# Kernel tuning notes

Measured on AMD Instinct MI355X. Metric: run time of the kernel, lower is better.

Reference implementation:

```python
import jax, jax.numpy as jnp
import numpy as np

EPS = 1e-6
NUM_GROUPS = 32


def group_norm(x, w, b):
    # x: [B, C, W, H, L]
    B, C = x.shape[0], x.shape[1]
    xr = x.reshape(B, NUM_GROUPS, C // NUM_GROUPS, -1)
    mu = jnp.mean(xr, axis=(2, 3), keepdims=True)
    var = jnp.var(xr, axis=(2, 3), keepdims=True)
    xn = ((xr - mu) * jax.lax.rsqrt(var + EPS)).reshape(x.shape)
    return xn * w[None, :, None, None, None] + b[None, :, None, None, None]


def setup_inputs() -> dict:
    key = jax.random.key(0)
    ks = jax.random.split(key, 8)
    B, C, W, H, L = 2, 512, 16, 16, 16
    s = 1.0 / np.sqrt(C)
    return {
        "x": jax.random.normal(ks[0], (B, C, W, H, L), dtype=jnp.float32),
        "gn_w": jnp.ones((C,), dtype=jnp.float32),
        "gn_b": jnp.zeros((C,), dtype=jnp.float32),
        "q_w": jax.random.normal(ks[1], (C, C), dtype=jnp.float32) * s,
        "q_b": jnp.zeros((C,), dtype=jnp.float32),
        "k_w": jax.random.normal(ks[2], (C, C), dtype=jnp.float32) * s,
        "k_b": jnp.zeros((C,), dtype=jnp.float32),
        "v_w": jax.random.normal(ks[3], (C, C), dtype=jnp.float32) * s,
        "v_b": jnp.zeros((C,), dtype=jnp.float32),
        "p_w": jax.random.normal(ks[4], (C, C), dtype=jnp.float32) * s,
        "p_b": jnp.zeros((C,), dtype=jnp.float32),
    }


def reference(x, gn_w, gn_b, q_w, q_b, k_w, k_b, v_w, v_b, p_w, p_b):
    B, C, W, H, L = x.shape
    h = group_norm(x, gn_w, gn_b)
    hf = h.reshape(B, C, -1)  # [B, C, N]
    # 1x1 Conv3d == channel matmul: out[b,o,n] = sum_c w[o,c] * h[b,c,n] + b[o]
    q = jnp.einsum('oc,bcn->bon', q_w, hf) + q_b[None, :, None]
    k = jnp.einsum('oc,bcn->bon', k_w, hf) + k_b[None, :, None]
    v = jnp.einsum('oc,bcn->bon', v_w, hf) + v_b[None, :, None]
    scale = jnp.asarray(C, x.dtype) ** -0.5
    # w_[b,i,j] = sum_c q[b,c,i] * k[b,c,j]
    w_ = jnp.einsum('bci,bcj->bij', q, k) * scale
    w_ = jax.nn.softmax(w_, axis=2)
    # h_[b,c,i] = sum_j v[b,c,j] * w_[b,i,j]
    attn = jnp.einsum('bcj,bij->bci', v, w_)
    proj = jnp.einsum('oc,bcn->bon', p_w, attn) + p_b[None, :, None]
    return x + proj.reshape(B, C, W, H, L)
```

## Files before the change

### kernel.cpp

```cpp
#include <hip/hip_runtime.h>


typedef __bf16 bf16;
typedef __attribute__((ext_vector_type(8))) __bf16 bf16x8;
typedef __attribute__((ext_vector_type(4))) __bf16 bf16x4;
typedef __attribute__((ext_vector_type(4))) float f32x4;

#define CC 512
#define NN 4096
#define BM 128
#define BN 128
#define BK 64
#define SCALE_L2E 0.06376237870903338f

__device__ __forceinline__ void gload16(const bf16* g, bf16* l) {
    __builtin_amdgcn_global_load_lds(
        (const __attribute__((address_space(1))) unsigned int*)g,
        (__attribute__((address_space(3))) unsigned int*)l, 16, 0, 0);
}

template<int FA, int NSTEP>
__device__ __forceinline__ void core_p3(
    const bf16* __restrict__ A, int lda,
    const bf16* __restrict__ B, int ldb,
    int m0, int n0, f32x4 acc[FA][2])
{
    constexpr int BMt  = FA * 32;
    constexpr int ROWS = BMt + 128;
    constexpr int L    = ROWS / 64;
    __shared__ __align__(16) bf16 ls[3][ROWS][BK];

    const int t    = threadIdx.x;
    const int lane = t & 63;
    const int wid  = t >> 6;
    const int wm   = (wid >> 2) * (FA * 16);
    const int wn   = (wid & 3) * 32;
    const int fr   = lane & 15;
    const int kq   = lane >> 4;
    const int cs0  = ((kq)     ^ (fr & 7)) * 8;
    const int cs1  = ((kq + 4) ^ (fr & 7)) * 8;

    auto STAGE = [&](int bi, int kk) {
        #pragma unroll
        for (int j = 0; j < L; ++j) {
            const int idx = t + j * 512;
            const int row = idx >> 3;
            const int blk = (idx & 7) ^ (row & 7);
            const bf16* g = (row < BMt)
                ? A + (size_t)(m0 + row) * lda + kk + blk * 8
                : B + (size_t)(n0 + row - BMt) * ldb + kk + blk * 8;
            gload16(g, &ls[bi][row][(idx & 7) * 8]);
        }
    };

    STAGE(0, 0);
    STAGE(1, BK);
    for (int i = 0; i < NSTEP; ++i) {
        if (i + 2 < NSTEP) {
            STAGE((i + 2) % 3, (i + 2) * BK);
            asm volatile("s_waitcnt vmcnt(%0)" :: "n"(2 * L) : "memory");
        } else if (i + 1 < NSTEP) {
            asm volatile("s_waitcnt vmcnt(%0)" :: "n"(L) : "memory");
        } else {
            asm volatile("s_waitcnt vmcnt(0)" ::: "memory");
        }
        __builtin_amdgcn_s_barrier();
        const int bi = i % 3;
        #pragma unroll
        for (int h = 0; h < 2; ++h) {
            const int cs = h ? cs1 : cs0;
            bf16x8 af[FA], bg[2];
            #pragma unroll
            for (int f = 0; f < FA; ++f)
                af[f] = *(const bf16x8*)&ls[bi][wm + f * 16 + fr][cs];
            #pragma unroll
            for (int g = 0; g < 2; ++g)
                bg[g] = *(const bf16x8*)&ls[bi][BMt + wn + g * 16 + fr][cs];
            #pragma unroll
            for (int fm = 0; fm < FA; ++fm)
                #pragma unroll
                for (int g = 0; g < 2; ++g)
                    acc[fm][g] = __builtin_amdgcn_mfma_f32_16x16x32_bf16(
                        af[fm], bg[g], acc[fm][g], 0, 0, 0);
        }
        __builtin_amdgcn_s_barrier();
    }
}

__device__ __forceinline__ void gemm_core(
    const bf16* __restrict__ A, int lda,
    const bf16* __restrict__ B, int ldb,
    int kBeg, int kEnd, int m0, int n0, f32x4 acc[4][4])
{
    __shared__ __align__(16) bf16 Als[2][BM][BK];
    __shared__ __align__(16) bf16 Bls[2][BN][BK];
    const int t    = threadIdx.x;
    const int lane = t & 63;
    const int wid  = t >> 6;
    const int wm   = (wid >> 1) * 64;
    const int wn   = (wid & 1) * 64;
    const int fr   = lane & 15;
    const int kq   = lane >> 4;
    const int r_   = t >> 3;
    const int cbs  = (t & 7) ^ (r_ & 7);
    const int dcol = (t & 7) * 8;
    const int cs0  = ((kq)     ^ (fr & 7)) * 8;
    const int cs1  = ((kq + 4) ^ (fr & 7)) * 8;

    const bf16* Ab = A + (size_t)(m0 + r_) * lda + cbs * 8;
    const bf16* Bb = B + (size_t)(n0 + r_) * ldb + cbs * 8;

#define STAGE_G(bufi, kk) do {                                              \
        _Pragma("unroll")                                                   \
        for (int i = 0; i < 4; ++i)                                         \
            gload16(Ab + (kk) + (size_t)(i * 32) * lda,                     \
                    &Als[bufi][i * 32 + r_][dcol]);                         \
        _Pragma("unroll")                                                   \
        for (int i = 0; i < 4; ++i)                                         \
            gload16(Bb + (kk) + (size_t)(i * 32) * ldb,                     \
                    &Bls[bufi][i * 32 + r_][dcol]);                         \
    } while (0)

    int cur = 0;
    STAGE_G(0, kBeg);
    __syncthreads();
    for (int k0 = kBeg; k0 < kEnd; k0 += BK) {
        if (k0 + BK < kEnd) STAGE_G(cur ^ 1, k0 + BK);
        #pragma unroll
        for (int h = 0; h < 2; ++h) {
            const int cs = h ? cs1 : cs0;
            bf16x8 af[4], bg[4];
            #pragma unroll
            for (int f = 0; f < 4; ++f) {
                af[f] = *(const bf16x8*)&Als[cur][wm + f * 16 + fr][cs];
                bg[f] = *(const bf16x8*)&Bls[cur][wn + f * 16 + fr][cs];
            }
            #pragma unroll
            for (int fm = 0; fm < 4; ++fm)
                #pragma unroll
                for (int fn = 0; fn < 4; ++fn)
                    acc[fm][fn] = __builtin_amdgcn_mfma_f32_16x16x32_bf16(
                        af[fm], bg[fn], acc[fm][fn], 0, 0, 0);
        }
        __syncthreads();
        cur ^= 1;
    }
#undef STAGE_G
}

__global__ __launch_bounds__(256) void convert_w_kernel(
    const float* __restrict__ qw, const float* __restrict__ kw,
    const float* __restrict__ pw, bf16* __restrict__ dst)
{
    const int which = blockIdx.y;
    const float* src = which == 0 ? qw : which == 1 ? kw : pw;
    const int slot  = which == 2 ? 3 : which;
    bf16* d = dst + (size_t)slot * (CC * CC);
    const int f4 = blockIdx.x * 256 + threadIdx.x;
    float4 v = ((const float4*)src)[f4];
    bf16x4 o;
    o[0] = (bf16)v.x; o[1] = (bf16)v.y; o[2] = (bf16)v.z; o[3] = (bf16)v.w;
    ((bf16x4*)d)[f4] = o;
}

__global__ __launch_bounds__(256) void vwT_kernel(
    const float* __restrict__ vw, bf16* __restrict__ vwT)
{
    const int k0 = blockIdx.x * 64;
    const int c0 = blockIdx.y * 64;
    const int t  = threadIdx.x;
    const int tk = t & 15, tc = t >> 4;
    float o[4][4];
    #pragma unroll
    for (int j = 0; j < 4; ++j) {
        const int c = c0 + tc * 4 + j;
        float4 v = *(const float4*)(vw + (size_t)c * CC + k0 + tk * 4);
        o[j][0] = v.x; o[j][1] = v.y; o[j][2] = v.z; o[j][3] = v.w;
    }
    #pragma unroll
    for (int i = 0; i < 4; ++i) {
        bf16x4 w4;
        w4[0] = (bf16)o[0][i]; w4[1] = (bf16)o[1][i];
        w4[2] = (bf16)o[2][i]; w4[3] = (bf16)o[3][i];
        *(bf16x4*)(vwT + (size_t)(k0 + tk * 4 + i) * CC + c0 + tc * 4) = w4;
    }
}

__global__ __launch_bounds__(256) void wb_kernel(
    const float* __restrict__ pw, const float* __restrict__ vb,
    float* __restrict__ wb)
{
    const int o = blockIdx.x * 256 + threadIdx.x;
    const float4* row = (const float4*)(pw + (size_t)o * CC);
    const float4* v4  = (const float4*)vb;
    float s = 0.f;
    #pragma unroll 4
    for (int i = 0; i < 128; ++i) {
        float4 a = row[i], b = v4[i];
        s += a.x * b.x + a.y * b.y + a.z * b.z + a.w * b.w;
    }
    wb[o] = s;
}

__global__ __launch_bounds__(256) void gn_stats_kernel(
    const float* __restrict__ x, float* __restrict__ mr)
{
    const int bg = blockIdx.x;
    const float4* base = (const float4*)(x + (size_t)bg * 16 * NN);
    const int t = threadIdx.x;
    float s = 0.f, sq = 0.f;
    #pragma unroll 4
    for (int i = 0; i < 64; ++i) {
        float4 v = base[i * 256 + t];
        s  += v.x + v.y + v.z + v.w;
        sq += v.x * v.x + v.y * v.y + v.z * v.z + v.w * v.w;
    }
    #pragma unroll
    for (int o = 32; o > 0; o >>= 1) { s += __shfl_xor(s, o); sq += __shfl_xor(sq, o); }
    __shared__ float rs[4], rq[4];
    const int lane = t & 63, wid = t >> 6;
    if (lane == 0) { rs[wid] = s; rq[wid] = sq; }
    __syncthreads();
    if (t == 0) {
        float S = rs[0] + rs[1] + rs[2] + rs[3];
        float Q = rq[0] + rq[1] + rq[2] + rq[3];
        const float invn = 1.f / 65536.f;
        float mean = S * invn;
        float var  = Q * invn - mean * mean;
        mr[bg * 2]     = mean;
        mr[bg * 2 + 1] = rsqrtf(var + 1e-6f);
    }
}

__global__ __launch_bounds__(256) void gn_apply_T_kernel(
    const float* __restrict__ x, const float* __restrict__ gw,
    const float* __restrict__ gb, const float* __restrict__ mr,
    bf16* __restrict__ hT)
{
    const int b  = blockIdx.z;
    const int n0 = blockIdx.x * 64;
    const int c0 = blockIdx.y * 64;
    const int t  = threadIdx.x;
    const int tn = t & 15, tc = t >> 4;
    float o[4][4];
    #pragma unroll
    for (int j = 0; j < 4; ++j) {
        const int c = c0 + tc * 4 + j;
        const int bg = b * 32 + (c >> 4);
        const float mean = mr[bg * 2], rstd = mr[bg * 2 + 1];
        const float w  = gw[c] * rstd;
        const float bb = gb[c] - mean * w;
        float4 v = *(const float4*)(x + ((size_t)(b * CC + c)) * NN + n0 + tn * 4);
        o[j][0] = v.x * w + bb; o[j][1] = v.y * w + bb;
        o[j][2] = v.z * w + bb; o[j][3] = v.w * w + bb;
    }
    bf16* dst = hT + (size_t)b * (size_t)NN * CC;
    #pragma unroll
    for (int i = 0; i < 4; ++i) {
        bf16x4 w4;
        w4[0] = (bf16)o[0][i]; w4[1] = (bf16)o[1][i];
        w4[2] = (bf16)o[2][i]; w4[3] = (bf16)o[3][i];
        *(bf16x4*)(dst + (size_t)(n0 + tn * 4 + i) * CC + c0 + tc * 4) = w4;
    }
}

__global__ __launch_bounds__(256) void fw_gemm_kernel(
    const bf16* __restrict__ pwb, const bf16* __restrict__ vwT,
    bf16* __restrict__ fw)
{
    const int m0 = blockIdx.y * BM, n0 = blockIdx.x * BN;
    f32x4 acc[4][4] = {};
    gemm_core(pwb, CC, vwT, CC, 0, CC, m0, n0, acc);
    const int lane = threadIdx.x & 63, wid = threadIdx.x >> 6;
    const int wm = (wid >> 1) * 64, wn = (wid & 1) * 64;
    const int cf = lane & 15, rb = (lane >> 4) * 4;
    #pragma unroll
    for (int fm = 0; fm < 4; ++fm)
      #pragma unroll
      for (int fn = 0; fn < 4; ++fn)
        #pragma unroll
        for (int r = 0; r < 4; ++r)
            fw[(size_t)(m0 + wm + fm * 16 + rb + r) * CC
               + (n0 + wn + fn * 16 + cf)] = (bf16)acc[fm][fn][r];
}

__global__ __launch_bounds__(512, 2) void qk_gemm_kernel(
    const bf16* __restrict__ hT, const bf16* __restrict__ wbf,
    const float* __restrict__ qb, const float* __restrict__ kb,
    bf16* __restrict__ qT, bf16* __restrict__ kT)
{
    const int z = blockIdx.z, b = z >> 1, w = z & 1;
    const size_t CN = (size_t)CC * NN;
    const bf16* A = hT + (size_t)b * CN;
    const bf16* B = wbf + (size_t)w * CC * CC;
    const float* bias = w ? kb : qb;
    bf16* outp = (w ? kT : qT) + (size_t)b * CN;
    const int m0 = blockIdx.y * 256, n0 = blockIdx.x * 128;
    f32x4 acc[8][2] = {};
    core_p3<8, CC / BK>(A, CC, B, CC, m0, n0, acc);
    const int lane = threadIdx.x & 63, wid = threadIdx.x >> 6;
    const int wm = (wid >> 2) * 128, wn = (wid & 3) * 32;
    const int cf = lane & 15, rb = (lane >> 4) * 4;
    #pragma unroll
    for (int fm = 0; fm < 8; ++fm)
      #pragma unroll
      for (int g = 0; g < 2; ++g)
        #pragma unroll
        for (int r = 0; r < 4; ++r) {
            int row = m0 + wm + fm * 16 + rb + r;
            int col = n0 + wn + g * 16 + cf;
            float val = acc[fm][g][r] + bias[col];
            if (w == 0) val *= SCALE_L2E;
            outp[(size_t)row * CC + col] = (bf16)val;
        }
}

__global__ __launch_bounds__(512, 2) void w_gemm_kernel(
    const bf16* __restrict__ fw, const bf16* __restrict__ hT,
    bf16* __restrict__ Wt)
{
    const int b = blockIdx.z;
    const size_t CN = (size_t)CC * NN;
    const int m0 = blockIdx.y * 128, n0 = blockIdx.x * 128;
    f32x4 acc[4][2] = {};
    core_p3<4, CC / BK>(fw, CC, hT + (size_t)b * CN, CC, m0, n0, acc);
    bf16* outp = Wt + (size_t)b * CN;
    const int lane = threadIdx.x & 63, wid = threadIdx.x >> 6;
    const int wm = (wid >> 2) * 64, wn = (wid & 3) * 32;
    const int cf = lane & 15, rb = (lane >> 4) * 4;
    #pragma unroll
    for (int fm = 0; fm < 4; ++fm)
      #pragma unroll
      for (int g = 0; g < 2; ++g)
        #pragma unroll
        for (int r = 0; r < 4; ++r)
            outp[(size_t)(m0 + wm + fm * 16 + rb + r) * NN
                 + (n0 + wn + g * 16 + cf)] = (bf16)acc[fm][g][r];
}

__global__ __launch_bounds__(512, 2) void se_gemm_kernel(
    const bf16* __restrict__ qT, const bf16* __restrict__ kT,
    bf16* __restrict__ E, float* __restrict__ rowsum)
{
    const int b = blockIdx.z;
    const size_t CN = (size_t)CC * NN;
    const bf16* qT_b = qT + (size_t)b * CN;
    const bf16* kT_b = kT + (size_t)b * CN;
    bf16* E_b = E + (size_t)b * NN * NN;
    float* rs_b = rowsum + (size_t)b * NN;
    const int m0 = blockIdx.y * 256, n0 = blockIdx.x * 128;
    f32x4 acc[8][2] = {};
    core_p3<8, CC / BK>(qT_b, CC, kT_b, CC, m0, n0, acc);
    const int lane = threadIdx.x & 63, wid = threadIdx.x >> 6;
    const int wm = (wid >> 2) * 128, wn = (wid & 3) * 32;
    const int cf = lane & 15, rb = (lane >> 4) * 4;
    #pragma unroll
    for (int fm = 0; fm < 8; ++fm)
      #pragma unroll
      for (int g = 0; g < 2; ++g)
        #pragma unroll
        for (int r = 0; r < 4; ++r) {
            float e = exp2f(fminf(acc[fm][g][r], 86.f));
            acc[fm][g][r] = e;
            E_b[(size_t)(m0 + wm + fm * 16 + rb + r) * NN
                + (n0 + wn + g * 16 + cf)] = (bf16)e;
        }
    #pragma unroll
    for (int fm = 0; fm < 8; ++fm)
      #pragma unroll
      for (int r = 0; r < 4; ++r) {
          float s = acc[fm][0][r] + acc[fm][1][r];
          s += __shfl_xor(s, 1); s += __shfl_xor(s, 2);
          s += __shfl_xor(s, 4); s += __shfl_xor(s, 8);
          if (cf == 0)
              atomicAdd(&rs_b[m0 + wm + fm * 16 + rb + r], s);
      }
}

__global__ __launch_bounds__(512, 2) void pvproj_kernel(
    const bf16* __restrict__ Wt, const bf16* __restrict__ E,
    const float* __restrict__ rowsum, const float* __restrict__ wb,
    const float* __restrict__ pb, const float* __restrict__ x,
    float* __restrict__ outp)
{
    const int b = blockIdx.z;
    const size_t CN = (size_t)CC * NN;
    const int m0 = blockIdx.y * 128, n0 = blockIdx.x * 128;
    f32x4 acc[4][2] = {};
    core_p3<4, NN / BK>(Wt + (size_t)b * CN, NN,
                        E + (size_t)b * NN * NN, NN, m0, n0, acc);
    const float* rs_b = rowsum + (size_t)b * NN;
    const int lane = threadIdx.x & 63, wid = threadIdx.x >> 6;
    const int wm = (wid >> 2) * 64, wn = (wid & 3) * 32;
    const int cf = lane & 15, rb = (lane >> 4) * 4;
    #pragma unroll
    for (int fm = 0; fm < 4; ++fm)
      #pragma unroll
      for (int g = 0; g < 2; ++g) {
          const int col = n0 + wn + g * 16 + cf;
          const float inv = 1.f / rs_b[col];
          #pragma unroll
          for (int r = 0; r < 4; ++r) {
              const int row = m0 + wm + fm * 16 + rb + r;
              const size_t idx = (size_t)b * CN + (size_t)row * NN + col;
              outp[idx] = acc[fm][g][r] * inv + wb[row] + pb[row] + x[idx];
          }
      }
}

extern "C" void kernel_launch(void* const* d_in, const int* in_sizes, int n_in,
                              void* d_out, int out_size, void* d_ws, size_t ws_size,
                              hipStream_t stream)
{
    const float* x   = (const float*)d_in[0];
    const float* gnw = (const float*)d_in[1];
    const float* gnb = (const float*)d_in[2];
    const float* qw  = (const float*)d_in[3];
    const float* qb  = (const float*)d_in[4];
    const float* kw  = (const float*)d_in[5];
    const float* kb  = (const float*)d_in[6];
    const float* vw  = (const float*)d_in[7];
    const float* vb  = (const float*)d_in[8];
    const float* pw  = (const float*)d_in[9];
    const float* pb  = (const float*)d_in[10];
    float* outp = (float*)d_out;

    char* ws = (char*)d_ws;
    size_t off = 0;
    auto alloc = [&](size_t bytes) -> char* {
        char* p = ws + off;
        off = (off + bytes + 255) & ~(size_t)255;
        return p;
    };
    const size_t CN = (size_t)CC * NN;
    bf16*  wbf  = (bf16*)alloc(4 * (size_t)CC * CC * sizeof(bf16));
    bf16*  hT   = (bf16*)alloc(2 * CN * sizeof(bf16));
    bf16*  qT   = (bf16*)alloc(2 * CN * sizeof(bf16));
    bf16*  kT   = (bf16*)alloc(2 * CN * sizeof(bf16));
    bf16*  fw   = (bf16*)alloc((size_t)CC * CC * sizeof(bf16));
    bf16*  Wt   = (bf16*)alloc(2 * CN * sizeof(bf16));
    bf16*  E    = (bf16*)alloc(2 * (size_t)NN * NN * sizeof(bf16));
    float* rowsum = (float*)alloc(2 * NN * sizeof(float));
    float* wb   = (float*)alloc(CC * sizeof(float));
    float* mr   = (float*)alloc(64 * 2 * sizeof(float));

    bf16* vwT = wbf + 2 * (size_t)CC * CC;
    bf16* pwb = wbf + 3 * (size_t)CC * CC;

    convert_w_kernel<<<dim3(256, 3), 256, 0, stream>>>(qw, kw, pw, wbf);
    vwT_kernel<<<dim3(8, 8), 256, 0, stream>>>(vw, vwT);
    wb_kernel<<<2, 256, 0, stream>>>(pw, vb, wb);
    gn_stats_kernel<<<64, 256, 0, stream>>>(x, mr);
    gn_apply_T_kernel<<<dim3(NN / 64, CC / 64, 2), 256, 0, stream>>>(
        x, gnw, gnb, mr, hT);
    hipMemsetAsync(rowsum, 0, 2 * NN * sizeof(float), stream);

    fw_gemm_kernel<<<dim3(4, 4), 256, 0, stream>>>(pwb, vwT, fw);
    qk_gemm_kernel<<<dim3(CC / 128, NN / 256, 4), 512, 0, stream>>>(
        hT, wbf, qb, kb, qT, kT);
    w_gemm_kernel<<<dim3(NN / 128, CC / 128, 2), 512, 0, stream>>>(fw, hT, Wt);

    se_gemm_kernel<<<dim3(NN / 128, NN / 256, 2), 512, 0, stream>>>(
        qT, kT, E, rowsum);

    pvproj_kernel<<<dim3(NN / 128, CC / 128, 2), 512, 0, stream>>>(
        Wt, E, rowsum, wb, pb, x, outp);
}
```

Baseline: 222.6 us.

## Use 256x256 GEMM tiles, merge QK/W GEMMs, split-K the PV projection

Replaces the triple-buffered variable-height GEMM core with a double-buffered 256x256 tile core giving each wave an 8x4 MFMA fragment block, for more reuse per LDS load. The Q, K and W projection GEMMs are fused into one launch that picks its role from the block index. The PV projection is split four ways along K and accumulates fp32 partials with atomics into a buffer that reuses the qT/kT space. Normalisation, biases and the residual are then applied in a separate elementwise pass. This trades extra memset, atomic and elementwise traffic, plus shallower pipelining, for larger tiles and better SM fill in the long-K GEMM.

```diff
diff --git a/kernel.cpp b/kernel.cpp
--- a/kernel.cpp
+++ b/kernel.cpp
@@ -8,8 +8,6 @@
 
 #define CC 512
 #define NN 4096
-#define BM 128
-#define BN 128
 #define BK 64
 #define SCALE_L2E 0.06376237870903338f
 
@@ -19,71 +17,84 @@
         (__attribute__((address_space(3))) unsigned int*)l, 16, 0, 0);
 }
 
-template<int FA, int NSTEP>
-__device__ __forceinline__ void core_p3(
+__device__ __forceinline__ void core256(
     const bf16* __restrict__ A, int lda,
     const bf16* __restrict__ B, int ldb,
-    int m0, int n0, f32x4 acc[FA][2])
-{
-    constexpr int BMt  = FA * 32;
-    constexpr int ROWS = BMt + 128;
-    constexpr int L    = ROWS / 64;
-    __shared__ __align__(16) bf16 ls[3][ROWS][BK];
+    int m0, int n0, int kBeg, int nt, f32x4 acc[8][4])
+{
+    __shared__ __align__(16) bf16 lsA[2][256][64];
+    __shared__ __align__(16) bf16 lsB[2][256][64];
 
     const int t    = threadIdx.x;
     const int lane = t & 63;
     const int wid  = t >> 6;
-    const int wm   = (wid >> 2) * (FA * 16);
-    const int wn   = (wid & 3) * 32;
+    const int wr   = wid >> 2;
+    const int wc   = wid & 3;
     const int fr   = lane & 15;
     const int kq   = lane >> 4;
     const int cs0  = ((kq)     ^ (fr & 7)) * 8;
     const int cs1  = ((kq + 4) ^ (fr & 7)) * 8;
 
-    auto STAGE = [&](int bi, int kk) {
+    const int r0  = t >> 3;
+    const int blk = (t & 7) ^ (r0 & 7);
+    const int dc  = (t & 7) * 8;
+    const bf16* Abase = A + (size_t)(m0 + r0) * lda + kBeg + blk * 8;
+    const bf16* Bbase = B + (size_t)(n0 + r0) * ldb + kBeg + blk * 8;
+
+    auto STAGE = [&](int db, int kk) {
+        const bf16* Ag = Abase + kk;
+        const bf16* Bg = Bbase + kk;
+        bf16* la = &lsA[db][r0][dc];
+        bf16* lb = &lsB[db][r0][dc];
         #pragma unroll
-        for (int j = 0; j < L; ++j) {
-            const int idx = t + j * 512;
-            const int row = idx >> 3;
-            const int blk = (idx & 7) ^ (row & 7);
-            const bf16* g = (row < BMt)
-                ? A + (size_t)(m0 + row) * lda + kk + blk * 8
-                : B + (size_t)(n0 + row - BMt) * ldb + kk + blk * 8;
-            gload16(g, &ls[bi][row][(idx & 7) * 8]);
+        for (int j = 0; j < 4; ++j)
+            gload16(Ag + (size_t)(64 * j) * lda, la + j * 64 * 64);
+        #pragma unroll
+        for (int j = 0; j < 4; ++j)
+            gload16(Bg + (size_t)(64 * j) * ldb, lb + j * 64 * 64);
+    };
+
+    STAGE(0, 0);
+    asm volatile("s_waitcnt vmcnt(0)" ::: "memory");
+    __builtin_amdgcn_s_barrier();
+    STAGE(1, BK);
+
+    const int arow = wr * 128 + fr;
+    const int brow = wc * 64 + fr;
+
+    for (int t_ = 0; t_ < nt; ++t_) {
+        const int db = t_ & 1;
+        const bf16 (*Ab)[64] = lsA[db];
+        const bf16 (*Bb)[64] = lsB[db];
+        #pragma unroll
+        for (int kh = 0; kh < 2; ++kh) {
+            const int cs = kh ? cs1 : cs0;
+            bf16x8 bgr[4];
+            #pragma unroll
+            for (int g = 0; g < 4; ++g)
+                bgr[g] = *(const bf16x8*)&Bb[brow + g * 16][cs];
+            #pragma unroll
+            for (int mh = 0; mh < 2; ++mh) {
+                bf16x8 afr[4];
+                #pragma unroll
+                for (int f = 0; f < 4; ++f)
+                    afr[f] = *(const bf16x8*)&Ab[arow + mh * 64 + f * 16][cs];
+                #pragma unroll
+                for (int f = 0; f < 4; ++f)
+                    #pragma unroll
+                    for (int g = 0; g < 4; ++g)
+                        acc[mh * 4 + f][g] = __builtin_amdgcn_mfma_f32_16x16x32_bf16(
+                            afr[f], bgr[g], acc[mh * 4 + f][g], 0, 0, 0);
+            }
         }
-    };
-
-    STAGE(0, 0);
-    STAGE(1, BK);
-    for (int i = 0; i < NSTEP; ++i) {
-        if (i + 2 < NSTEP) {
-            STAGE((i + 2) % 3, (i + 2) * BK);
-            asm volatile("s_waitcnt vmcnt(%0)" :: "n"(2 * L) : "memory");
-        } else if (i + 1 < NSTEP) {
-            asm volatile("s_waitcnt vmcnt(%0)" :: "n"(L) : "memory");
+        __builtin_amdgcn_s_barrier();
+        if (t_ + 2 < nt) {
+            STAGE(db, (t_ + 2) * BK);
+            asm volatile("s_waitcnt vmcnt(8)" ::: "memory");
         } else {
             asm volatile("s_waitcnt vmcnt(0)" ::: "memory");
         }
         __builtin_amdgcn_s_barrier();
-        const int bi = i % 3;
-        #pragma unroll
-        for (int h = 0; h < 2; ++h) {
-            const int cs = h ? cs1 : cs0;
-            bf16x8 af[FA], bg[2];
-            #pragma unroll
-            for (int f = 0; f < FA; ++f)
-                af[f] = *(const bf16x8*)&ls[bi][wm + f * 16 + fr][cs];
-            #pragma unroll
-            for (int g = 0; g < 2; ++g)
-                bg[g] = *(const bf16x8*)&ls[bi][BMt + wn + g * 16 + fr][cs];
-            #pragma unroll
-            for (int fm = 0; fm < FA; ++fm)
-                #pragma unroll
-                for (int g = 0; g < 2; ++g)
-                    acc[fm][g] = __builtin_amdgcn_mfma_f32_16x16x32_bf16(
-                        af[fm], bg[g], acc[fm][g], 0, 0, 0);
-        }
-        __builtin_amdgcn_s_barrier();
     }
 }
 
@@ -92,8 +103,8 @@
     const bf16* __restrict__ B, int ldb,
     int kBeg, int kEnd, int m0, int n0, f32x4 acc[4][4])
 {
-    __shared__ __align__(16) bf16 Als[2][BM][BK];
-    __shared__ __align__(16) bf16 Bls[2][BN][BK];
+    __shared__ __align__(16) bf16 Als[2][128][BK];
+    __shared__ __align__(16) bf16 Bls[2][128][BK];
     const int t    = threadIdx.x;
     const int lane = t & 63;
     const int wid  = t >> 6;
@@ -268,7 +279,7 @@
     const bf16* __restrict__ pwb, const bf16* __restrict__ vwT,
     bf16* __restrict__ fw)
 {
-    const int m0 = blockIdx.y * BM, n0 = blockIdx.x * BN;
+    const int m0 = blockIdx.y * 128, n0 = blockIdx.x * 128;
     f32x4 acc[4][4] = {};
     gemm_core(pwb, CC, vwT, CC, 0, CC, m0, n0, acc);
     const int lane = threadIdx.x & 63, wid = threadIdx.x >> 6;
@@ -284,58 +295,53 @@
                + (n0 + wn + fn * 16 + cf)] = (bf16)acc[fm][fn][r];
 }
 
-__global__ __launch_bounds__(512, 2) void qk_gemm_kernel(
+__global__ __launch_bounds__(512, 2) void qkw_gemm_kernel(
     const bf16* __restrict__ hT, const bf16* __restrict__ wbf,
+    const bf16* __restrict__ fw,
     const float* __restrict__ qb, const float* __restrict__ kb,
-    bf16* __restrict__ qT, bf16* __restrict__ kT)
-{
-    const int z = blockIdx.z, b = z >> 1, w = z & 1;
+    bf16* __restrict__ qT, bf16* __restrict__ kT, bf16* __restrict__ Wt)
+{
+    const int b = blockIdx.z;
     const size_t CN = (size_t)CC * NN;
-    const bf16* A = hT + (size_t)b * CN;
-    const bf16* B = wbf + (size_t)w * CC * CC;
-    const float* bias = w ? kb : qb;
-    bf16* outp = (w ? kT : qT) + (size_t)b * CN;
-    const int m0 = blockIdx.y * 256, n0 = blockIdx.x * 128;
-    f32x4 acc[8][2] = {};
-    core_p3<8, CC / BK>(A, CC, B, CC, m0, n0, acc);
+    const int x = blockIdx.x;
+    const int role = x >> 5, s = x & 31;
+    const bf16* hT_b = hT + (size_t)b * CN;
+
+    const bf16* A; int lda; const bf16* B; int ldb;
+    int m0, n0, ldo; bf16* outp; const float* bias;
+    if (role < 2) {
+        A = hT_b; lda = CC;
+        B = wbf + (size_t)role * CC * CC; ldb = CC;
+        m0 = (s >> 1) * 256; n0 = (s & 1) * 256;
+        outp = (role ? kT : qT) + (size_t)b * CN; ldo = CC;
+        bias = role ? kb : qb;
+    } else {
+        A = fw; lda = CC;
+        B = hT_b; ldb = CC;
+        m0 = (s >> 4) * 256; n0 = (s & 15) * 256;
+        outp = Wt + (size_t)b * CN; ldo = NN;
+        bias = nullptr;
+    }
+    f32x4 acc[8][4] = {};
+    core256(A, lda, B, ldb, m0, n0, 0, CC / BK, acc);
+
     const int lane = threadIdx.x & 63, wid = threadIdx.x >> 6;
-    const int wm = (wid >> 2) * 128, wn = (wid & 3) * 32;
+    const int wr = wid >> 2, wc = wid & 3;
     const int cf = lane & 15, rb = (lane >> 4) * 4;
     #pragma unroll
     for (int fm = 0; fm < 8; ++fm)
       #pragma unroll
-      for (int g = 0; g < 2; ++g)
-        #pragma unroll
-        for (int r = 0; r < 4; ++r) {
-            int row = m0 + wm + fm * 16 + rb + r;
-            int col = n0 + wn + g * 16 + cf;
-            float val = acc[fm][g][r] + bias[col];
-            if (w == 0) val *= SCALE_L2E;
-            outp[(size_t)row * CC + col] = (bf16)val;
-        }
-}
-
-__global__ __launch_bounds__(512, 2) void w_gemm_kernel(
-    const bf16* __restrict__ fw, const bf16* __restrict__ hT,
-    bf16* __restrict__ Wt)
-{
-    const int b = blockIdx.z;
-    const size_t CN = (size_t)CC * NN;
-    const int m0 = blockIdx.y * 128, n0 = blockIdx.x * 128;
-    f32x4 acc[4][2] = {};
-    core_p3<4, CC / BK>(fw, CC, hT + (size_t)b * CN, CC, m0, n0, acc);
-    bf16* outp = Wt + (size_t)b * CN;
-    const int lane = threadIdx.x & 63, wid = threadIdx.x >> 6;
-    const int wm = (wid >> 2) * 64, wn = (wid & 3) * 32;
-    const int cf = lane & 15, rb = (lane >> 4) * 4;
-    #pragma unroll
-    for (int fm = 0; fm < 4; ++fm)
-      #pragma unroll
-      for (int g = 0; g < 2; ++g)
-        #pragma unroll
-        for (int r = 0; r < 4; ++r)
-            outp[(size_t)(m0 + wm + fm * 16 + rb + r) * NN
-                 + (n0 + wn + g * 16 + cf)] = (bf16)acc[fm][g][r];
+      for (int g = 0; g < 4; ++g) {
+          const int col = n0 + wc * 64 + g * 16 + cf;
+          const float bv = (role < 2) ? bias[col] : 0.f;
+          #pragma unroll
+          for (int r = 0; r < 4; ++r) {
+              const int row = m0 + wr * 128 + fm * 16 + rb + r;
+              float val = acc[fm][g][r] + bv;
+              if (role == 0) val *= SCALE_L2E;
+              outp[(size_t)row * ldo + col] = (bf16)val;
+          }
+      }
 }
 
 __global__ __launch_bounds__(512, 2) void se_gemm_kernel(
@@ -348,64 +354,91 @@
     const bf16* kT_b = kT + (size_t)b * CN;
     bf16* E_b = E + (size_t)b * NN * NN;
     float* rs_b = rowsum + (size_t)b * NN;
-    const int m0 = blockIdx.y * 256, n0 = blockIdx.x * 128;
-    f32x4 acc[8][2] = {};
-    core_p3<8, CC / BK>(qT_b, CC, kT_b, CC, m0, n0, acc);
+    const int m0 = blockIdx.y * 256, n0 = blockIdx.x * 256;
+    f32x4 acc[8][4] = {};
+    core256(qT_b, CC, kT_b, CC, m0, n0, 0, CC / BK, acc);
+
     const int lane = threadIdx.x & 63, wid = threadIdx.x >> 6;
-    const int wm = (wid >> 2) * 128, wn = (wid & 3) * 32;
+    const int wr = wid >> 2, wc = wid & 3;
     const int cf = lane & 15, rb = (lane >> 4) * 4;
     #pragma unroll
     for (int fm = 0; fm < 8; ++fm)
       #pragma unroll
-      for (int g = 0; g < 2; ++g)
+      for (int g = 0; g < 4; ++g)
         #pragma unroll
         for (int r = 0; r < 4; ++r) {
             float e = exp2f(fminf(acc[fm][g][r], 86.f));
             acc[fm][g][r] = e;
-            E_b[(size_t)(m0 + wm + fm * 16 + rb + r) * NN
-                + (n0 + wn + g * 16 + cf)] = (bf16)e;
+            E_b[(size_t)(m0 + wr * 128 + fm * 16 + rb + r) * NN
+                + (n0 + wc * 64 + g * 16 + cf)] = (bf16)e;
         }
     #pragma unroll
     for (int fm = 0; fm < 8; ++fm)
       #pragma unroll
       for (int r = 0; r < 4; ++r) {
-          float s = acc[fm][0][r] + acc[fm][1][r];
+          float s = acc[fm][0][r] + acc[fm][1][r] + acc[fm][2][r] + acc[fm][3][r];
           s += __shfl_xor(s, 1); s += __shfl_xor(s, 2);
           s += __shfl_xor(s, 4); s += __shfl_xor(s, 8);
           if (cf == 0)
-              atomicAdd(&rs_b[m0 + wm + fm * 16 + rb + r], s);
+              atomicAdd(&rs_b[m0 + wr * 128 + fm * 16 + rb + r], s);
       }
 }
 
 __global__ __launch_bounds__(512, 2) void pvproj_kernel(
     const bf16* __restrict__ Wt, const bf16* __restrict__ E,
-    const float* __restrict__ rowsum, const float* __restrict__ wb,
-    const float* __restrict__ pb, const float* __restrict__ x,
-    float* __restrict__ outp)
-{
-    const int b = blockIdx.z;
+    float* __restrict__ S32)
+{
+    const int b  = blockIdx.z >> 2;
+    const int ks = blockIdx.z & 3;
     const size_t CN = (size_t)CC * NN;
-    const int m0 = blockIdx.y * 128, n0 = blockIdx.x * 128;
-    f32x4 acc[4][2] = {};
-    core_p3<4, NN / BK>(Wt + (size_t)b * CN, NN,
-                        E + (size_t)b * NN * NN, NN, m0, n0, acc);
-    const float* rs_b = rowsum + (size_t)b * NN;
+    const int m0 = blockIdx.y * 256, n0 = blockIdx.x * 256;
+    f32x4 acc[8][4] = {};
+    core256(Wt + (size_t)b * CN, NN, E + (size_t)b * NN * NN, NN,
+            m0, n0, ks * 1024, 16, acc);
+    float* S_b = S32 + (size_t)b * CN;
     const int lane = threadIdx.x & 63, wid = threadIdx.x >> 6;
-    const int wm = (wid >> 2) * 64, wn = (wid & 3) * 32;
+    const int wr = wid >> 2, wc = wid & 3;
     const int cf = lane & 15, rb = (lane >> 4) * 4;
     #pragma unroll
-    for (int fm = 0; fm < 4; ++fm)
+    for (int fm = 0; fm < 8; ++fm)
       #pragma unroll
-      for (int g = 0; g < 2; ++g) {
-          const int col = n0 + wn + g * 16 + cf;
-          const float inv = 1.f / rs_b[col];
+      for (int g = 0; g < 4; ++g) {
+          const int col = n0 + wc * 64 + g * 16 + cf;
           #pragma unroll
           for (int r = 0; r < 4; ++r) {
-              const int row = m0 + wm + fm * 16 + rb + r;
-              const size_t idx = (size_t)b * CN + (size_t)row * NN + col;
-              outp[idx] = acc[fm][g][r] * inv + wb[row] + pb[row] + x[idx];
+              const int row = m0 + wr * 128 + fm * 16 + rb + r;
+              atomicAdd(&S_b[(size_t)row * NN + col], acc[fm][g][r]);
           }
       }
+}
+
+__global__ __launch_bounds__(256) void rsinv_kernel(
+    const float* __restrict__ rowsum, float* __restrict__ rsinv)
+{
+    const int i = blockIdx.x * 256 + threadIdx.x;
+    rsinv[i] = 1.f / rowsum[i];
+}
+
+__global__ __launch_bounds__(256) void pvfin_kernel(
+    const float* __restrict__ S32, const float* __restrict__ rsinv,
+    const float* __restrict__ wb, const float* __restrict__ pb,
+    const float* __restrict__ x, float* __restrict__ outp)
+{
+    const size_t f4 = (size_t)blockIdx.x * 256 + threadIdx.x;
+    const size_t e  = f4 * 4;
+    const int n = (int)(e & (NN - 1));
+    const int o = (int)((e >> 12) & (CC - 1));
+    const int b = (int)(e >> 21);
+    float4 sv = ((const float4*)S32)[f4];
+    float4 iv = *(const float4*)(rsinv + (size_t)b * NN + n);
+    float4 xv = ((const float4*)x)[f4];
+    const float bias = wb[o] + pb[o];
+    float4 ov;
+    ov.x = sv.x * iv.x + bias + xv.x;
+    ov.y = sv.y * iv.y + bias + xv.y;
+    ov.z = sv.z * iv.z + bias + xv.z;
+    ov.w = sv.w * iv.w + bias + xv.w;
+    ((float4*)outp)[f4] = ov;
 }
 
 extern "C" void kernel_launch(void* const* d_in, const int* in_sizes, int n_in,
@@ -441,8 +474,10 @@
     bf16*  Wt   = (bf16*)alloc(2 * CN * sizeof(bf16));
     bf16*  E    = (bf16*)alloc(2 * (size_t)NN * NN * sizeof(bf16));
     float* rowsum = (float*)alloc(2 * NN * sizeof(float));
+    float* rsinv  = (float*)alloc(2 * NN * sizeof(float));
     float* wb   = (float*)alloc(CC * sizeof(float));
     float* mr   = (float*)alloc(64 * 2 * sizeof(float));
+    float* S32  = (float*)qT;
 
     bf16* vwT = wbf + 2 * (size_t)CC * CC;
     bf16* pwb = wbf + 3 * (size_t)CC * CC;
@@ -456,13 +491,14 @@
     hipMemsetAsync(rowsum, 0, 2 * NN * sizeof(float), stream);
 
     fw_gemm_kernel<<<dim3(4, 4), 256, 0, stream>>>(pwb, vwT, fw);
-    qk_gemm_kernel<<<dim3(CC / 128, NN / 256, 4), 512, 0, stream>>>(
-        hT, wbf, qb, kb, qT, kT);
-    w_gemm_kernel<<<dim3(NN / 128, CC / 128, 2), 512, 0, stream>>>(fw, hT, Wt);
-
-    se_gemm_kernel<<<dim3(NN / 128, NN / 256, 2), 512, 0, stream>>>(
-        qT, kT, E, rowsum);
-
-    pvproj_kernel<<<dim3(NN / 128, CC / 128, 2), 512, 0, stream>>>(
-        Wt, E, rowsum, wb, pb, x, outp);
-}
+    qkw_gemm_kernel<<<dim3(96, 1, 2), 512, 0, stream>>>(
+        hT, wbf, fw, qb, kb, qT, kT, Wt);
+
+    se_gemm_kernel<<<dim3(16, 16, 2), 512, 0, stream>>>(qT, kT, E, rowsum);
+
+    rsinv_kernel<<<32, 256, 0, stream>>>(rowsum, rsinv);
+    hipMemsetAsync(S32, 0, 2 * CN * sizeof(float), stream);
+    pvproj_kernel<<<dim3(16, 2, 8), 512, 0, stream>>>(Wt, E, S32);
+
+    pvfin_kernel<<<4096, 256, 0, stream>>>(S32, rsinv, wb, pb, x, outp);
+}
```

Measured after the change: 245.4 us. 10.3% more time.
